# Performance work log

Measured on AMD Instinct MI355X. Metric: run time of the kernel, lower is better.

## Reference

```python
import jax, jax.numpy as jnp
import numpy as np

D_MODEL = 1536
N_HEADS = 12
HEAD_DIM = D_MODEL // N_HEADS  # 128
H_GROUP = N_HEADS // 3         # 4
B, T = 2, 2048
ROPE_THETA = 1000000.0
EPS = 1.1920928955078125e-07   # torch.finfo(float32).eps (nn.RMSNorm default)


def setup_inputs() -> dict:
    key = jax.random.key(0)
    ks = jax.random.split(key, 12)
    pdim = H_GROUP * HEAD_DIM
    s_in = 1.0 / np.sqrt(D_MODEL)
    inp = {"hidden_states": jax.random.normal(ks[0], (B, T, D_MODEL), jnp.float32)}
    names = ["wq_f", "wk_f", "wv_f", "wq_b", "wk_b", "wv_b", "wq_d", "wk_d", "wv_d"]
    for i, n in enumerate(names):
        inp[n] = jax.random.normal(ks[1 + i], (pdim, D_MODEL), jnp.float32) * s_in
    inp["wo"] = jax.random.normal(ks[10], (D_MODEL, N_HEADS * HEAD_DIM), jnp.float32) * s_in
    inp["q_norm_w"] = jnp.ones((HEAD_DIM,), jnp.float32)
    inp["k_norm_w"] = jnp.ones((HEAD_DIM,), jnp.float32)
    ii = jnp.arange(T)
    inp["forward_mask"] = ii[:, None] >= ii[None, :]   # causal
    inp["backward_mask"] = ii[:, None] <= ii[None, :]  # anti-causal
    inp["bidirectional_mask"] = jnp.ones((T, T), bool)
    return inp


def _rmsnorm(x, w):
    return x * jax.lax.rsqrt(jnp.mean(x * x, axis=-1, keepdims=True) + EPS) * w


def _rotate_half(x):
    x1, x2 = jnp.split(x, 2, axis=-1)
    return jnp.concatenate([-x2, x1], axis=-1)


def _rope_tables(seq_len):
    inv_freq = 1.0 / (ROPE_THETA ** (jnp.arange(0, HEAD_DIM, 2, dtype=jnp.float32) / HEAD_DIM))
    freqs = jnp.outer(jnp.arange(seq_len, dtype=jnp.float32), inv_freq)
    emb = jnp.concatenate([freqs, freqs], axis=-1)  # [T, head_dim]
    return jnp.cos(emb), jnp.sin(emb)


def _project_rope(x, wq, wk, wv, q_norm_w, k_norm_w, cos, sin):
    Bq, Tq, _ = x.shape
    def proj(w):
        return (x @ w.T).reshape(Bq, Tq, H_GROUP, HEAD_DIM).transpose(0, 2, 1, 3)
    q, k, v = proj(wq), proj(wk), proj(wv)
    q = _rmsnorm(q, q_norm_w)
    k = _rmsnorm(k, k_norm_w)
    c = cos[None, None]  # [1,1,T,hd]
    s = sin[None, None]
    q = q * c + _rotate_half(q) * s
    k = k * c + _rotate_half(k) * s
    return q, k, v


def _attn(q, k, v, mask):
    scale = 1.0 / np.sqrt(HEAD_DIM)
    scores = jnp.einsum("bhqd,bhkd->bhqk", q, k) * scale
    scores = jnp.where(mask[None, None], scores, -jnp.inf)
    w = jax.nn.softmax(scores, axis=-1)
    return jnp.einsum("bhqk,bhkd->bhqd", w, v)


def reference(hidden_states, wq_f, wk_f, wv_f, wq_b, wk_b, wv_b, wq_d, wk_d, wv_d,
              wo, q_norm_w, k_norm_w, forward_mask, backward_mask, bidirectional_mask):
    Bq, Tq, _ = hidden_states.shape
    cos, sin = _rope_tables(Tq)
    outs = []
    for (wq, wk, wv, m) in [(wq_f, wk_f, wv_f, forward_mask),
                            (wq_b, wk_b, wv_b, backward_mask),
                            (wq_d, wk_d, wv_d, bidirectional_mask)]:
        q, k, v = _project_rope(hidden_states, wq, wk, wv, q_norm_w, k_norm_w, cos, sin)
        a = _attn(q, k, v, m)  # [B,h,T,hd]
        outs.append(a.transpose(0, 2, 1, 3).reshape(Bq, Tq, H_GROUP * HEAD_DIM))
    attn_concat = jnp.concatenate(outs, axis=-1)
    return attn_concat @ wo.T
```

## Files before the change

### kernel.cpp

```cpp
#include <hip/hip_runtime.h>
#include <stdint.h>
#include <stddef.h>

typedef __attribute__((ext_vector_type(8))) short bf16x8;
typedef __attribute__((ext_vector_type(4))) float f32x4;

#define DMODEL 1536
#define TSEQ   2048
#define HDIM   128
#define NBR    3
#define NHB    4
#define MROWS  4096

__device__ __forceinline__ float bf2f(unsigned short u) {
  union { unsigned int i; float f; } v; v.i = ((unsigned int)u) << 16; return v.f;
}
__device__ __forceinline__ unsigned short f2bf(float f) {
  union { float f; unsigned int i; } v; v.f = f;
  unsigned int r = v.i + 0x7fffu + ((v.i >> 16) & 1u);
  return (unsigned short)(r >> 16);
}
__device__ __forceinline__ unsigned int cvtpk(float lo, float hi) {
  unsigned int r;
  asm("v_cvt_pk_bf16_f32 %0, %1, %2" : "=v"(r) : "v"(lo), "v"(hi));
  return r;
}
__device__ __forceinline__ void gload_lds16(const void* g, void* l) {
  __builtin_amdgcn_global_load_lds((__attribute__((address_space(1))) void*)g,
                                   (__attribute__((address_space(3))) void*)l,
                                   16, 0, 0);
}

__global__ __launch_bounds__(256) void k_cvt(const float* __restrict__ src,
                                             unsigned short* __restrict__ dst,
                                             int n4) {
  int i = blockIdx.x * 256 + threadIdx.x;
  if (i >= n4) return;
  float4 v = ((const float4*)src)[i];
  ushort4 o;
  o.x = f2bf(v.x); o.y = f2bf(v.y); o.z = f2bf(v.z); o.w = f2bf(v.w);
  ((ushort4*)dst)[i] = o;
}

struct W9 { const float* w[9]; };

__global__ __launch_bounds__(256) void k_cvt9(W9 ws, unsigned short* __restrict__ dst,
                                              int n4) {
  int seg = blockIdx.y;
  const float* __restrict__ src = ws.w[seg];
  unsigned short* __restrict__ d = dst + (size_t)seg * (size_t)n4 * 4;
  int i = blockIdx.x * 256 + threadIdx.x;
  if (i >= n4) return;
  float4 v = ((const float4*)src)[i];
  ushort4 o;
  o.x = f2bf(v.x); o.y = f2bf(v.y); o.z = f2bf(v.z); o.w = f2bf(v.w);
  ((ushort4*)d)[i] = o;
}

#define GBM 128
#define GBN 192
#define GBK 64
#define GK  1536
#define GNT (GK / GBK)

template<int EPI>
__global__ __launch_bounds__(512, 4) void k_gemm8(
    const unsigned short* __restrict__ A, const unsigned short* __restrict__ Bw,
    unsigned short* __restrict__ Qs, unsigned short* __restrict__ Ksl,
    unsigned short* __restrict__ Vs, float* __restrict__ Cout)
{
  __shared__ __align__(16) unsigned short As[2 * GBM * GBK];
  __shared__ __align__(16) unsigned short Bs[2 * GBN * GBK];

  const int t = threadIdx.x, ln = t & 63, w = t >> 6;
  const int wm = w >> 2, wn = w & 3, g = ln >> 4, li = ln & 15;

  const int nwg = gridDim.x * gridDim.y;
  const int lid = blockIdx.y * gridDim.x + blockIdx.x;
  const int s = (lid & 7) * (nwg >> 3) + (lid >> 3);
  const int m0 = (s & 31) * GBM;
  const int n0 = (s >> 5) * GBN;

  f32x4 zero4 = {0.f, 0.f, 0.f, 0.f};
  f32x4 acc[4][3];
#pragma unroll
  for (int i = 0; i < 4; ++i)
#pragma unroll
    for (int j = 0; j < 3; ++j) acc[i][j] = zero4;

  auto STAGE = [&](int p, int kt) {
    const unsigned short* Ag = A + (size_t)m0 * GK + kt * GBK;
    unsigned short* Al = As + p * (GBM * GBK);
#pragma unroll
    for (int i = 0; i < 2; ++i) {
      int ch = i * 512 + t; int r = ch >> 3, c = ch & 7;
      gload_lds16(Ag + (size_t)r * GK + ((c ^ (r & 7)) * 8), Al + ch * 8);
    }
    const unsigned short* Bg = Bw + (size_t)n0 * GK + kt * GBK;
    unsigned short* Bl = Bs + p * (GBN * GBK);
#pragma unroll
    for (int i = 0; i < 3; ++i) {
      int ch = i * 512 + t; int r = ch >> 3, c = ch & 7;
      gload_lds16(Bg + (size_t)r * GK + ((c ^ (r & 7)) * 8), Bl + ch * 8);
    }
  };

  STAGE(0, 0);
  STAGE(1, 1);

  for (int kt = 0; kt < GNT; ++kt) {
    const int cur = kt & 1;
    if (kt < GNT - 1) { asm volatile("s_waitcnt vmcnt(5)" ::: "memory"); }
    else              { asm volatile("s_waitcnt vmcnt(0)" ::: "memory"); }
    __builtin_amdgcn_sched_barrier(0);
    __builtin_amdgcn_s_barrier();
    __builtin_amdgcn_sched_barrier(0);
    asm volatile("" ::: "memory");

    const unsigned short* Al = As + cur * (GBM * GBK);
    const unsigned short* Bl = Bs + cur * (GBN * GBK);
#pragma unroll
    for (int kh = 0; kh < 2; ++kh) {
      bf16x8 af[4], bfn[3];
#pragma unroll
      for (int mf = 0; mf < 4; ++mf) {
        int r = wm * 64 + mf * 16 + li;
        af[mf] = *(const bf16x8*)(Al + r * 64 + (((kh * 4 + g) ^ (li & 7)) * 8));
      }
#pragma unroll
      for (int nf = 0; nf < 3; ++nf) {
        int r = wn * 48 + nf * 16 + li;
        bfn[nf] = *(const bf16x8*)(Bl + r * 64 + (((kh * 4 + g) ^ (li & 7)) * 8));
      }
      __builtin_amdgcn_s_setprio(1);
#pragma unroll
      for (int mf = 0; mf < 4; ++mf)
#pragma unroll
        for (int nf = 0; nf < 3; ++nf)
          acc[mf][nf] = __builtin_amdgcn_mfma_f32_16x16x32_bf16(
              af[mf], bfn[nf], acc[mf][nf], 0, 0, 0);
      __builtin_amdgcn_s_setprio(0);
    }
    asm volatile("" ::: "memory");
    __builtin_amdgcn_sched_barrier(0);
    __builtin_amdgcn_s_barrier();
    __builtin_amdgcn_sched_barrier(0);
    if (kt + 2 < GNT) STAGE(cur, kt + 2);
  }

#pragma unroll
  for (int mf = 0; mf < 4; ++mf)
#pragma unroll
    for (int nf = 0; nf < 3; ++nf)
#pragma unroll
      for (int rr = 0; rr < 4; ++rr) {
        int row = m0 + wm * 64 + mf * 16 + g * 4 + rr;
        int col = n0 + wn * 48 + nf * 16 + li;
        if (EPI == 0) {
          int mat = col >> 9, within = col & 511;
          int br = mat / 3, qkv = mat % 3;
          int b = row >> 11, tt = row & 2047;
          int h = within >> 7, d = within & 127;
          unsigned short* dst = (qkv == 0) ? Qs : (qkv == 1) ? Ksl : Vs;
          size_t off = ((size_t)((br * 2 + b) * 4 + h) * TSEQ + tt) * HDIM + d;
          dst[off] = f2bf(acc[mf][nf][rr]);
        } else {
          Cout[(size_t)row * DMODEL + col] = acc[mf][nf][rr];
        }
      }
}

__global__ __launch_bounds__(256) void k_rope(
    unsigned short* __restrict__ Q, unsigned short* __restrict__ K,
    const float* __restrict__ qw, const float* __restrict__ kw)
{
  const int t = threadIdx.x, ln = t & 63, w = t >> 6;
  const int rid = blockIdx.x * 4 + w;
  const int tt  = rid & (TSEQ - 1);
  const size_t base = (size_t)rid * HDIM;

  const float ang = (float)tt * exp2f(-0.31143075464f * (float)ln);
  float s, c;
  sincosf(ang, &s, &c);

#pragma unroll
  for (int which = 0; which < 2; ++which) {
    unsigned short* P = which ? K : Q;
    const float* Wn = which ? kw : qw;
    float x1 = bf2f(P[base + ln]);
    float x2 = bf2f(P[base + 64 + ln]);
    float ss = x1 * x1 + x2 * x2;
#pragma unroll
    for (int off = 1; off < 64; off <<= 1) ss += __shfl_xor(ss, off, 64);
    float rr = rsqrtf(ss * (1.0f / 128.0f) + 1.1920928955078125e-07f);
    float y1 = x1 * rr * Wn[ln];
    float y2 = x2 * rr * Wn[64 + ln];
    P[base + ln]      = f2bf(y1 * c - y2 * s);
    P[base + 64 + ln] = f2bf(y2 * c + y1 * s);
  }
}

__global__ __launch_bounds__(256) void k_vtrans(
    const unsigned short* __restrict__ V, unsigned short* __restrict__ VT)
{
  __shared__ unsigned short L[64 * 65];
  const int tb = blockIdx.x;
  const int db = blockIdx.y;
  const int sl = blockIdx.z;
  const size_t slab = (size_t)sl * (TSEQ * HDIM);
  const int t = threadIdx.x;

#pragma unroll
  for (int i = 0; i < 2; ++i) {
    int c = i * 256 + t;
    int trow = c >> 3, d0 = (c & 7) * 8;
    bf16x8 vv = *(const bf16x8*)(V + slab + (size_t)(tb*64 + trow) * HDIM + db*64 + d0);
#pragma unroll
    for (int j = 0; j < 8; ++j) L[trow * 65 + d0 + j] = (unsigned short)vv[j];
  }
  __syncthreads();
#pragma unroll
  for (int i = 0; i < 2; ++i) {
    int c = i * 256 + t;
    int drow = c >> 3, t0 = (c & 7) * 8;
    bf16x8 ov;
#pragma unroll
    for (int j = 0; j < 8; ++j) ov[j] = (short)L[(t0 + j) * 65 + drow];
    *(bf16x8*)(VT + slab + (size_t)(db*64 + drow) * TSEQ + tb*64 + t0) = ov;
  }
}

#define ATT_SCALE 0.08838834764831845f

template<int MODE>
__device__ __forceinline__ void flash_phase(
    int qt, int bh,
    const unsigned short* __restrict__ Q, const unsigned short* __restrict__ K,
    const unsigned short* __restrict__ VT, unsigned short* __restrict__ AO,
    unsigned short* SH)
{
  unsigned short* Ks = SH;
  unsigned short* Vt = SH + 8704;
  unsigned int*   Pl = (unsigned int*)(SH + 17920);

  const int b = bh >> 2, h = bh & 3;
  const int t = threadIdx.x, ln = t & 63, w = t >> 6;
  const int g = ln >> 4, li = ln & 15;
  const size_t slab = (size_t)(MODE * 8 + bh) * (TSEQ * HDIM);
  const int q0 = qt * 128;

  bf16x8 qf[4];
  {
    const unsigned short* qp = Q + slab + (size_t)(q0 + w*16 + li) * HDIM + g*8;
#pragma unroll
    for (int s = 0; s < 4; ++s) qf[s] = *(const bf16x8*)(qp + s * 32);
  }

  f32x4 zero4 = {0.f, 0.f, 0.f, 0.f};
  f32x4 acc_o[8];
#pragma unroll
  for (int fd = 0; fd < 8; ++fd) acc_o[fd] = zero4;
  float m_run = -1e30f, l_run = 0.f;

  const int kt0 = (MODE == 1) ? 2 * qt : 0;
  const int kt1 = (MODE == 0) ? 2 * qt + 1 : 31;
  unsigned int* Plw = Pl + w * (16 * 36);

  bf16x8 rk0, rk1, rv0, rv1;
  const int krA = t >> 4,          kcA = (t & 15) * 8;
  const int krB = 32 + (t >> 4);
  const int vdA = t >> 3,          vtA = (t & 7) * 8;
  const int vdB = 64 + (t >> 3);

  auto LOADT = [&](int kt) {
    const int k0 = kt * 64;
    rk0 = *(const bf16x8*)(K + slab + (size_t)(k0 + krA) * HDIM + kcA);
    rk1 = *(const bf16x8*)(K + slab + (size_t)(k0 + krB) * HDIM + kcA);
    rv0 = *(const bf16x8*)(VT + slab + (size_t)vdA * TSEQ + k0 + vtA);
    rv1 = *(const bf16x8*)(VT + slab + (size_t)vdB * TSEQ + k0 + vtA);
  };

  LOADT(kt0);

  for (int kt = kt0; kt <= kt1; ++kt) {
    const int k0 = kt * 64;
    __syncthreads();

    *(bf16x8*)(Ks + krA * 136 + kcA) = rk0;
    *(bf16x8*)(Ks + krB * 136 + kcA) = rk1;
    *(bf16x8*)(Vt + vdA * 72 + vtA) = rv0;
    *(bf16x8*)(Vt + vdB * 72 + vtA) = rv1;

    if (kt < kt1) LOADT(kt + 1);

    __syncthreads();

    f32x4 sf[4];
#pragma unroll
    for (int fc = 0; fc < 4; ++fc) sf[fc] = zero4;
#pragma unroll
    for (int s = 0; s < 4; ++s) {
      bf16x8 kf[4];
#pragma unroll
      for (int fc = 0; fc < 4; ++fc)
        kf[fc] = *(const bf16x8*)(Ks + (fc*16 + li) * 136 + s*32 + g*8);
      __builtin_amdgcn_s_setprio(1);
#pragma unroll
      for (int fc = 0; fc < 4; ++fc)
        sf[fc] = __builtin_amdgcn_mfma_f32_16x16x32_bf16(kf[fc], qf[s], sf[fc], 0, 0, 0);
      __builtin_amdgcn_s_setprio(0);
    }

    const bool diag = (MODE == 0) ? (kt >= 2 * qt)
                    : (MODE == 1) ? (kt <= 2 * qt + 1) : false;
    float pf[16];
#pragma unroll
    for (int fc = 0; fc < 4; ++fc)
#pragma unroll
      for (int r = 0; r < 4; ++r) {
        float sv = sf[fc][r] * ATT_SCALE;
        if (diag) {
          int kg = k0 + fc*16 + g*4 + r;
          int qg = q0 + w*16 + li;
          bool ok = (MODE == 0) ? (kg <= qg) : (kg >= qg);
          sv = ok ? sv : -1e30f;
        }
        pf[fc*4 + r] = sv;
      }

    float x0 = fmaxf(fmaxf(pf[0],  pf[1]),  fmaxf(pf[2],  pf[3]));
    float x1 = fmaxf(fmaxf(pf[4],  pf[5]),  fmaxf(pf[6],  pf[7]));
    float x2 = fmaxf(fmaxf(pf[8],  pf[9]),  fmaxf(pf[10], pf[11]));
    float x3 = fmaxf(fmaxf(pf[12], pf[13]), fmaxf(pf[14], pf[15]));
    float m = fmaxf(fmaxf(x0, x1), fmaxf(x2, x3));
    m = fmaxf(m, __shfl_xor(m, 16, 64));
    m = fmaxf(m, __shfl_xor(m, 32, 64));

    if (__any(m > m_run)) {
      float mn = fmaxf(m_run, m);
      float alpha = __expf(m_run - mn);
      m_run = mn;
      l_run *= alpha;
#pragma unroll
      for (int fd = 0; fd < 8; ++fd) acc_o[fd] *= alpha;
    }

#pragma unroll
    for (int i = 0; i < 16; ++i) pf[i] = __expf(pf[i] - m_run);
    float s0 = (pf[0]  + pf[1])  + (pf[2]  + pf[3]);
    float s1 = (pf[4]  + pf[5])  + (pf[6]  + pf[7]);
    float s2 = (pf[8]  + pf[9])  + (pf[10] + pf[11]);
    float s3 = (pf[12] + pf[13]) + (pf[14] + pf[15]);
    float rs = (s0 + s1) + (s2 + s3);
    rs += __shfl_xor(rs, 16, 64);
    rs += __shfl_xor(rs, 32, 64);
    l_run += rs;

#pragma unroll
    for (int fc = 0; fc < 4; ++fc) {
      uint2 dwv;
      dwv.x = cvtpk(pf[fc*4 + 0], pf[fc*4 + 1]);
      dwv.y = cvtpk(pf[fc*4 + 2], pf[fc*4 + 3]);
      *(uint2*)(Plw + li*36 + fc*8 + g*2) = dwv;
    }
    asm volatile("s_waitcnt lgkmcnt(0)" ::: "memory");
    __builtin_amdgcn_sched_barrier(0);

#pragma unroll
    for (int ks = 0; ks < 2; ++ks) {
      bf16x8 pa = *(const bf16x8*)(Plw + li*36 + ks*16 + g*4);
      __builtin_amdgcn_s_setprio(1);
#pragma unroll
      for (int fd = 0; fd < 8; ++fd) {
        bf16x8 vb = *(const bf16x8*)(Vt + (fd*16 + li) * 72 + ks*32 + g*8);
        acc_o[fd] = __builtin_amdgcn_mfma_f32_16x16x32_bf16(vb, pa, acc_o[fd], 0, 0, 0);
      }
      __builtin_amdgcn_s_setprio(0);
    }
  }

  __syncthreads();
  unsigned short* ep = SH + w * 2176;
  unsigned int* epw = (unsigned int*)ep;
  float inv = 1.0f / l_run;
#pragma unroll
  for (int fd = 0; fd < 8; ++fd) {
    epw[li*68 + fd*8 + g*2 + 0] = cvtpk(acc_o[fd][0]*inv, acc_o[fd][1]*inv);
    epw[li*68 + fd*8 + g*2 + 1] = cvtpk(acc_o[fd][2]*inv, acc_o[fd][3]*inv);
  }
  asm volatile("s_waitcnt lgkmcnt(0)" ::: "memory");
  __builtin_amdgcn_sched_barrier(0);
  {
    const int ql = ln >> 2, sg = ln & 3;
    size_t rowbase = ((size_t)b * TSEQ + q0 + w*16 + ql) * DMODEL + MODE * 512 + h * HDIM;
#pragma unroll
    for (int rr = 0; rr < 4; ++rr) {
      bf16x8 v = *(const bf16x8*)(ep + ql*136 + sg*8 + rr*32);
      *(bf16x8*)(AO + rowbase + sg*8 + rr*32) = v;
    }
  }
}

__global__ __launch_bounds__(512, 2) void k_attn(
    const unsigned short* __restrict__ Q, const unsigned short* __restrict__ K,
    const unsigned short* __restrict__ VT, unsigned short* __restrict__ AO)
{
  __shared__ __align__(16) unsigned short SH[27136];

  const int qt = blockIdx.x;
  const int bh = blockIdx.y;
  if (blockIdx.z == 0) {
    flash_phase<0>(qt, bh, Q, K, VT, AO, SH);
    flash_phase<1>(qt, bh, Q, K, VT, AO, SH);
  } else {
    flash_phase<2>(qt, bh, Q, K, VT, AO, SH);
  }
}

extern "C" void kernel_launch(void* const* d_in, const int* in_sizes, int n_in,
                              void* d_out, int out_size, void* d_ws, size_t ws_size,
                              hipStream_t stream)
{
  (void)in_sizes; (void)n_in; (void)out_size; (void)ws_size;
  const float* Xf  = (const float*)d_in[0];
  const float* WOf = (const float*)d_in[10];
  const float* qw  = (const float*)d_in[11];
  const float* kw  = (const float*)d_in[12];

  const size_t S = (size_t)NBR * 2 * NHB * TSEQ * HDIM;
  unsigned short* Qs   = (unsigned short*)d_ws;
  unsigned short* Ks   = Qs + S;
  unsigned short* Vs   = Ks + S;
  unsigned short* AO   = Vs + S;
  unsigned short* Xbf  = AO + S;
  unsigned short* Wbf  = Xbf + (size_t)MROWS * DMODEL;
  unsigned short* WObf = Wbf + (size_t)9 * 512 * DMODEL;
  unsigned short* VTs  = Xbf;
  float* Cout = (float*)d_out;

  dim3 blk(256);

  k_cvt<<<dim3((MROWS * DMODEL) / 1024), blk, 0, stream>>>(Xf, Xbf, (MROWS * DMODEL) / 4);
  W9 w9;
  for (int i = 0; i < 9; ++i) w9.w[i] = (const float*)d_in[1 + i];
  k_cvt9<<<dim3((512 * DMODEL) / 1024, 9), blk, 0, stream>>>(w9, Wbf, (512 * DMODEL) / 4);
  k_cvt<<<dim3((DMODEL * DMODEL) / 1024), blk, 0, stream>>>(WOf, WObf, (DMODEL * DMODEL) / 4);

  k_gemm8<0><<<dim3(32, 24), dim3(512), 0, stream>>>(Xbf, Wbf, Qs, Ks, Vs, nullptr);
  k_rope<<<dim3(12288), blk, 0, stream>>>(Qs, Ks, qw, kw);
  k_vtrans<<<dim3(32, 2, 24), blk, 0, stream>>>(Vs, VTs);
  k_attn<<<dim3(16, 8, 2), dim3(512), 0, stream>>>(Qs, Ks, VTs, AO);
  k_gemm8<1><<<dim3(32, 8), dim3(512), 0, stream>>>(AO, WObf, nullptr, nullptr, nullptr, Cout);
}
```

Baseline: 207.5 us.

## Split KV loop across two wave groups with 32x32 MFMA and merged softmax

The attention phase now splits the 512-thread block into two 4-wave groups that process alternating 64-key tiles, each with its own K/V shared-memory slab. At the end they merge partial outputs through LDS using their running max and sum. QK and PV use 32x32x16 bf16 MFMAs, and P is built in registers with v_permlane32_swap instead of a round trip through LDS. This is meant to raise MFMA efficiency and per-wave work and to remove the P staging. In exchange it uses more LDS, adds a cross-group reduction epilogue with extra barriers, and raises register pressure from 32-lane accumulators.

```diff
diff --git a/kernel.cpp b/kernel.cpp
--- a/kernel.cpp
+++ b/kernel.cpp
@@ -4,6 +4,7 @@
 
 typedef __attribute__((ext_vector_type(8))) short bf16x8;
 typedef __attribute__((ext_vector_type(4))) float f32x4;
+typedef __attribute__((ext_vector_type(16))) float f32x16;
 
 #define DMODEL 1536
 #define TSEQ   2048
@@ -24,6 +25,9 @@
   unsigned int r;
   asm("v_cvt_pk_bf16_f32 %0, %1, %2" : "=v"(r) : "v"(lo), "v"(hi));
   return r;
+}
+__device__ __forceinline__ void plswap(unsigned int& a, unsigned int& b) {
+  asm("v_permlane32_swap_b32 %0, %1" : "+v"(a), "+v"(b));
 }
 __device__ __forceinline__ void gload_lds16(const void* g, void* l) {
   __builtin_amdgcn_global_load_lds((__attribute__((address_space(1))) void*)g,
@@ -239,101 +243,93 @@
     const unsigned short* __restrict__ VT, unsigned short* __restrict__ AO,
     unsigned short* SH)
 {
-  unsigned short* Ks = SH;
-  unsigned short* Vt = SH + 8704;
-  unsigned int*   Pl = (unsigned int*)(SH + 17920);
-
   const int b = bh >> 2, h = bh & 3;
-  const int t = threadIdx.x, ln = t & 63, w = t >> 6;
-  const int g = ln >> 4, li = ln & 15;
+  const int t = threadIdx.x, l = t & 63, w = t >> 6;
+  const int hi = l >> 5, l31 = l & 31;
+  const int wq = w & 3, gid = w >> 2;
   const size_t slab = (size_t)(MODE * 8 + bh) * (TSEQ * HDIM);
   const int q0 = qt * 128;
 
-  bf16x8 qf[4];
+  unsigned short* KsG = SH + gid * 17920;
+  unsigned short* VtG = KsG + 8704;
+
+  bf16x8 qf[8];
   {
-    const unsigned short* qp = Q + slab + (size_t)(q0 + w*16 + li) * HDIM + g*8;
-#pragma unroll
-    for (int s = 0; s < 4; ++s) qf[s] = *(const bf16x8*)(qp + s * 32);
-  }
-
-  f32x4 zero4 = {0.f, 0.f, 0.f, 0.f};
-  f32x4 acc_o[8];
-#pragma unroll
-  for (int fd = 0; fd < 8; ++fd) acc_o[fd] = zero4;
+    const unsigned short* qp = Q + slab + (size_t)(q0 + wq*32 + l31) * HDIM + hi*8;
+#pragma unroll
+    for (int st = 0; st < 8; ++st) qf[st] = *(const bf16x8*)(qp + st*16);
+  }
+
+  f32x16 zero16;
+#pragma unroll
+  for (int e = 0; e < 16; ++e) zero16[e] = 0.f;
+  f32x16 acc[4];
+#pragma unroll
+  for (int df = 0; df < 4; ++df) acc[df] = zero16;
   float m_run = -1e30f, l_run = 0.f;
 
-  const int kt0 = (MODE == 1) ? 2 * qt : 0;
-  const int kt1 = (MODE == 0) ? 2 * qt + 1 : 31;
-  unsigned int* Plw = Pl + w * (16 * 36);
-
-  bf16x8 rk0, rk1, rv0, rv1;
-  const int krA = t >> 4,          kcA = (t & 15) * 8;
-  const int krB = 32 + (t >> 4);
-  const int vdA = t >> 3,          vtA = (t & 7) * 8;
-  const int vdB = 64 + (t >> 3);
-
+  int n, ktbase, diagAt;
+  if (MODE == 0)      { n = qt + 1;  ktbase = gid;          diagAt = n - 1; }
+  else if (MODE == 1) { n = 16 - qt; ktbase = 2*qt + gid;   diagAt = 0; }
+  else                { n = 16;      ktbase = gid;          diagAt = -1; }
+
+  const int tl = t & 255;
+  bf16x8 rk[4], rv[4];
   auto LOADT = [&](int kt) {
     const int k0 = kt * 64;
-    rk0 = *(const bf16x8*)(K + slab + (size_t)(k0 + krA) * HDIM + kcA);
-    rk1 = *(const bf16x8*)(K + slab + (size_t)(k0 + krB) * HDIM + kcA);
-    rv0 = *(const bf16x8*)(VT + slab + (size_t)vdA * TSEQ + k0 + vtA);
-    rv1 = *(const bf16x8*)(VT + slab + (size_t)vdB * TSEQ + k0 + vtA);
+#pragma unroll
+    for (int j = 0; j < 4; ++j) {
+      int c = j * 256 + tl;
+      rk[j] = *(const bf16x8*)(K  + slab + (size_t)(k0 + (c >> 4)) * HDIM + (c & 15) * 8);
+      rv[j] = *(const bf16x8*)(VT + slab + (size_t)(c >> 3) * TSEQ + k0 + (c & 7) * 8);
+    }
   };
 
-  LOADT(kt0);
-
-  for (int kt = kt0; kt <= kt1; ++kt) {
+  LOADT(ktbase);
+
+  for (int i = 0; i < n; ++i) {
+    const int kt = ktbase + 2 * i;
     const int k0 = kt * 64;
     __syncthreads();
-
-    *(bf16x8*)(Ks + krA * 136 + kcA) = rk0;
-    *(bf16x8*)(Ks + krB * 136 + kcA) = rk1;
-    *(bf16x8*)(Vt + vdA * 72 + vtA) = rv0;
-    *(bf16x8*)(Vt + vdB * 72 + vtA) = rv1;
-
-    if (kt < kt1) LOADT(kt + 1);
-
+#pragma unroll
+    for (int j = 0; j < 4; ++j) {
+      int c = j * 256 + tl;
+      *(bf16x8*)(KsG + (c >> 4) * 136 + (c & 15) * 8) = rk[j];
+      *(bf16x8*)(VtG + (c >> 3) * 72  + (c & 7) * 8)  = rv[j];
+    }
+    if (i + 1 < n) LOADT(kt + 2);
     __syncthreads();
 
-    f32x4 sf[4];
-#pragma unroll
-    for (int fc = 0; fc < 4; ++fc) sf[fc] = zero4;
-#pragma unroll
-    for (int s = 0; s < 4; ++s) {
-      bf16x8 kf[4];
-#pragma unroll
-      for (int fc = 0; fc < 4; ++fc)
-        kf[fc] = *(const bf16x8*)(Ks + (fc*16 + li) * 136 + s*32 + g*8);
+    f32x16 sf0 = zero16, sf1 = zero16;
+#pragma unroll
+    for (int st = 0; st < 8; ++st) {
+      bf16x8 kf0 = *(const bf16x8*)(KsG + l31 * 136 + st*16 + hi*8);
+      bf16x8 kf1 = *(const bf16x8*)(KsG + (32 + l31) * 136 + st*16 + hi*8);
       __builtin_amdgcn_s_setprio(1);
-#pragma unroll
-      for (int fc = 0; fc < 4; ++fc)
-        sf[fc] = __builtin_amdgcn_mfma_f32_16x16x32_bf16(kf[fc], qf[s], sf[fc], 0, 0, 0);
+      sf0 = __builtin_amdgcn_mfma_f32_32x32x16_bf16(kf0, qf[st], sf0, 0, 0, 0);
+      sf1 = __builtin_amdgcn_mfma_f32_32x32x16_bf16(kf1, qf[st], sf1, 0, 0, 0);
       __builtin_amdgcn_s_setprio(0);
     }
 
-    const bool diag = (MODE == 0) ? (kt >= 2 * qt)
-                    : (MODE == 1) ? (kt <= 2 * qt + 1) : false;
-    float pf[16];
-#pragma unroll
-    for (int fc = 0; fc < 4; ++fc)
-#pragma unroll
-      for (int r = 0; r < 4; ++r) {
-        float sv = sf[fc][r] * ATT_SCALE;
-        if (diag) {
-          int kg = k0 + fc*16 + g*4 + r;
-          int qg = q0 + w*16 + li;
+    float pf[32];
+#pragma unroll
+    for (int r = 0; r < 16; ++r) { pf[r] = sf0[r] * ATT_SCALE; pf[16+r] = sf1[r] * ATT_SCALE; }
+
+    if (MODE != 2 && i == diagAt) {
+      const int qg = q0 + wq*32 + l31;
+#pragma unroll
+      for (int f = 0; f < 2; ++f)
+#pragma unroll
+        for (int r = 0; r < 16; ++r) {
+          int kg = k0 + f*32 + 4*hi + (r & 3) + 8*(r >> 2);
           bool ok = (MODE == 0) ? (kg <= qg) : (kg >= qg);
-          sv = ok ? sv : -1e30f;
+          if (!ok) pf[f*16 + r] = -1e30f;
         }
-        pf[fc*4 + r] = sv;
-      }
-
-    float x0 = fmaxf(fmaxf(pf[0],  pf[1]),  fmaxf(pf[2],  pf[3]));
-    float x1 = fmaxf(fmaxf(pf[4],  pf[5]),  fmaxf(pf[6],  pf[7]));
-    float x2 = fmaxf(fmaxf(pf[8],  pf[9]),  fmaxf(pf[10], pf[11]));
-    float x3 = fmaxf(fmaxf(pf[12], pf[13]), fmaxf(pf[14], pf[15]));
-    float m = fmaxf(fmaxf(x0, x1), fmaxf(x2, x3));
-    m = fmaxf(m, __shfl_xor(m, 16, 64));
+    }
+
+    float m = pf[0];
+#pragma unroll
+    for (int j = 1; j < 32; ++j) m = fmaxf(m, pf[j]);
     m = fmaxf(m, __shfl_xor(m, 32, 64));
 
     if (__any(m > m_run)) {
@@ -342,61 +338,105 @@
       m_run = mn;
       l_run *= alpha;
 #pragma unroll
-      for (int fd = 0; fd < 8; ++fd) acc_o[fd] *= alpha;
-    }
-
-#pragma unroll
-    for (int i = 0; i < 16; ++i) pf[i] = __expf(pf[i] - m_run);
-    float s0 = (pf[0]  + pf[1])  + (pf[2]  + pf[3]);
-    float s1 = (pf[4]  + pf[5])  + (pf[6]  + pf[7]);
-    float s2 = (pf[8]  + pf[9])  + (pf[10] + pf[11]);
-    float s3 = (pf[12] + pf[13]) + (pf[14] + pf[15]);
-    float rs = (s0 + s1) + (s2 + s3);
-    rs += __shfl_xor(rs, 16, 64);
+      for (int df = 0; df < 4; ++df) acc[df] *= alpha;
+    }
+
+    float rs0 = 0.f, rs1 = 0.f, rs2 = 0.f, rs3 = 0.f;
+#pragma unroll
+    for (int j = 0; j < 8; ++j) { pf[j]      = __expf(pf[j]      - m_run); rs0 += pf[j]; }
+#pragma unroll
+    for (int j = 8; j < 16; ++j){ pf[j]      = __expf(pf[j]      - m_run); rs1 += pf[j]; }
+#pragma unroll
+    for (int j = 0; j < 8; ++j) { pf[16+j]   = __expf(pf[16+j]   - m_run); rs2 += pf[16+j]; }
+#pragma unroll
+    for (int j = 8; j < 16; ++j){ pf[16+j]   = __expf(pf[16+j]   - m_run); rs3 += pf[16+j]; }
+    float rs = (rs0 + rs1) + (rs2 + rs3);
     rs += __shfl_xor(rs, 32, 64);
     l_run += rs;
 
-#pragma unroll
-    for (int fc = 0; fc < 4; ++fc) {
-      uint2 dwv;
-      dwv.x = cvtpk(pf[fc*4 + 0], pf[fc*4 + 1]);
-      dwv.y = cvtpk(pf[fc*4 + 2], pf[fc*4 + 3]);
-      *(uint2*)(Plw + li*36 + fc*8 + g*2) = dwv;
-    }
-    asm volatile("s_waitcnt lgkmcnt(0)" ::: "memory");
-    __builtin_amdgcn_sched_barrier(0);
-
-#pragma unroll
-    for (int ks = 0; ks < 2; ++ks) {
-      bf16x8 pa = *(const bf16x8*)(Plw + li*36 + ks*16 + g*4);
-      __builtin_amdgcn_s_setprio(1);
-#pragma unroll
-      for (int fd = 0; fd < 8; ++fd) {
-        bf16x8 vb = *(const bf16x8*)(Vt + (fd*16 + li) * 72 + ks*32 + g*8);
-        acc_o[fd] = __builtin_amdgcn_mfma_f32_16x16x32_bf16(vb, pa, acc_o[fd], 0, 0, 0);
-      }
-      __builtin_amdgcn_s_setprio(0);
+    unsigned int pb[2][8];
+#pragma unroll
+    for (int f = 0; f < 2; ++f) {
+#pragma unroll
+      for (int u = 0; u < 4; ++u) {
+        pb[f][2*u]   = cvtpk(pf[f*16 + 4*u + 0], pf[f*16 + 4*u + 1]);
+        pb[f][2*u+1] = cvtpk(pf[f*16 + 4*u + 2], pf[f*16 + 4*u + 3]);
+      }
+      plswap(pb[f][0], pb[f][2]);
+      plswap(pb[f][1], pb[f][3]);
+      plswap(pb[f][4], pb[f][6]);
+      plswap(pb[f][5], pb[f][7]);
+    }
+
+#pragma unroll
+    for (int s = 0; s < 4; ++s) {
+      union { unsigned int u[4]; bf16x8 v; } pbv;
+#pragma unroll
+      for (int u = 0; u < 4; ++u) pbv.u[u] = pb[s >> 1][(s & 1) * 4 + u];
+#pragma unroll
+      for (int df = 0; df < 4; ++df) {
+        bf16x8 vb = *(const bf16x8*)(VtG + (df*32 + l31) * 72 + s*16 + hi*8);
+        __builtin_amdgcn_s_setprio(1);
+        acc[df] = __builtin_amdgcn_mfma_f32_32x32x16_bf16(vb, pbv.v, acc[df], 0, 0, 0);
+        __builtin_amdgcn_s_setprio(0);
+      }
     }
   }
 
   __syncthreads();
-  unsigned short* ep = SH + w * 2176;
-  unsigned int* epw = (unsigned int*)ep;
-  float inv = 1.0f / l_run;
-#pragma unroll
-  for (int fd = 0; fd < 8; ++fd) {
-    epw[li*68 + fd*8 + g*2 + 0] = cvtpk(acc_o[fd][0]*inv, acc_o[fd][1]*inv);
-    epw[li*68 + fd*8 + g*2 + 1] = cvtpk(acc_o[fd][2]*inv, acc_o[fd][3]*inv);
-  }
-  asm volatile("s_waitcnt lgkmcnt(0)" ::: "memory");
-  __builtin_amdgcn_sched_barrier(0);
+  float* EXf = (float*)SH;
+  float* MLf = (float*)(SH + 35840);
+  if (gid == 1) {
+    MLf[(wq*64 + l)*2 + 0] = m_run;
+    MLf[(wq*64 + l)*2 + 1] = l_run;
+#pragma unroll
+    for (int df = 0; df < 4; ++df)
+#pragma unroll
+      for (int u = 0; u < 4; ++u) {
+        f32x4 ch = {acc[df][4*u], acc[df][4*u+1], acc[df][4*u+2], acc[df][4*u+3]};
+        *(f32x4*)&EXf[(wq*64 + l)*68 + df*16 + u*4] = ch;
+      }
+  }
+  __syncthreads();
+  if (gid == 0) {
+    float mB = MLf[(wq*64 + l)*2 + 0];
+    float lB = MLf[(wq*64 + l)*2 + 1];
+    float mF = fmaxf(m_run, mB);
+    float a0 = __expf(m_run - mF), a1 = __expf(mB - mF);
+    float inv = 1.0f / (l_run * a0 + lB * a1);
+    a0 *= inv; a1 *= inv;
+#pragma unroll
+    for (int df = 0; df < 4; ++df)
+#pragma unroll
+      for (int u = 0; u < 4; ++u) {
+        f32x4 cb = *(const f32x4*)&EXf[(wq*64 + l)*68 + df*16 + u*4];
+#pragma unroll
+        for (int e = 0; e < 4; ++e)
+          acc[df][4*u+e] = acc[df][4*u+e] * a0 + cb[e] * a1;
+      }
+  }
+  __syncthreads();
+
+  unsigned int* OT = (unsigned int*)SH;
+  if (gid == 0) {
+#pragma unroll
+    for (int df = 0; df < 4; ++df)
+#pragma unroll
+      for (int u = 0; u < 4; ++u) {
+        unsigned int d0 = cvtpk(acc[df][4*u+0], acc[df][4*u+1]);
+        unsigned int d1 = cvtpk(acc[df][4*u+2], acc[df][4*u+3]);
+        uint2 dd; dd.x = d0; dd.y = d1;
+        *(uint2*)&OT[(wq*32 + l31)*68 + df*16 + 2*hi + 4*u] = dd;
+      }
+  }
+  __syncthreads();
   {
-    const int ql = ln >> 2, sg = ln & 3;
-    size_t rowbase = ((size_t)b * TSEQ + q0 + w*16 + ql) * DMODEL + MODE * 512 + h * HDIM;
-#pragma unroll
-    for (int rr = 0; rr < 4; ++rr) {
-      bf16x8 v = *(const bf16x8*)(ep + ql*136 + sg*8 + rr*32);
-      *(bf16x8*)(AO + rowbase + sg*8 + rr*32) = v;
+    const int q = t >> 2, sg = t & 3;
+    size_t rowbase = ((size_t)b * TSEQ + q0 + q) * DMODEL + MODE * 512 + h * HDIM;
+#pragma unroll
+    for (int u = 0; u < 4; ++u) {
+      bf16x8 vv = *(const bf16x8*)&OT[q*68 + u*16 + sg*4];
+      *(bf16x8*)(AO + rowbase + (u*16 + sg*4)*2) = vv;
     }
   }
 }
@@ -405,7 +445,7 @@
     const unsigned short* __restrict__ Q, const unsigned short* __restrict__ K,
     const unsigned short* __restrict__ VT, unsigned short* __restrict__ AO)
 {
-  __shared__ __align__(16) unsigned short SH[27136];
+  __shared__ __align__(16) unsigned short SH[36864];
 
   const int qt = blockIdx.x;
   const int bh = blockIdx.y;
```

Result: faster. 191.6 us (-7.7%).
